# Performance work log

Hardware: AMD Instinct MI355X
Metric: run time of the kernel (lower is better)

## Reference

```python
import math
import jax, jax.numpy as jnp
import numpy as np

B, S, D, H = 2, 2048, 2048, 16
HD = D // H
INV_NORM = 1.0 / math.sqrt(HD)


def _build_alibi(batch, n_heads, seq_len):
    # Standard BLOOM ALiBi slopes (n_heads is a power of two here)
    base = 2.0 ** (-(2.0 ** -(math.log2(n_heads) - 3)))
    slopes = base ** np.arange(1, n_heads + 1, dtype=np.float32)  # [H]
    pos = np.arange(seq_len, dtype=np.float32)  # [S]
    alibi = slopes[:, None] * pos[None, :]  # [H, S]
    alibi = np.broadcast_to(alibi[None], (batch, n_heads, seq_len)).reshape(batch * n_heads, 1, seq_len)
    return jnp.asarray(alibi)


def _build_causal_mask(batch, seq_len):
    neg = jnp.float32(-1e9)
    tril = jnp.tril(jnp.ones((seq_len, seq_len), dtype=bool))
    mask = jnp.where(tril, jnp.float32(0.0), neg)  # [S, S]
    return jnp.broadcast_to(mask[None, None], (batch, 1, seq_len, seq_len))


def setup_inputs() -> dict:
    key = jax.random.key(0)
    ks = jax.random.split(key, 6)
    scale = 0.02
    return {
        "hidden_states": jax.random.normal(ks[0], (B, S, D), jnp.float32),
        "residual": jax.random.normal(ks[1], (B, S, D), jnp.float32),
        "alibi": _build_alibi(B, H, S),
        "attention_mask": _build_causal_mask(B, S),
        "W_qkv": jax.random.normal(ks[2], (3 * D, D), jnp.float32) * scale,
        "b_qkv": jax.random.normal(ks[3], (3 * D,), jnp.float32) * scale,
        "W_dense": jax.random.normal(ks[4], (D, D), jnp.float32) * scale,
        "b_dense": jax.random.normal(ks[5], (D,), jnp.float32) * scale,
    }


def reference(hidden_states, residual, alibi, attention_mask, W_qkv, b_qkv, W_dense, b_dense):
    b, s, d = hidden_states.shape
    # fused QKV projection: [B,S,3D] -> [B,S,H,3,HD]
    fused = (hidden_states @ W_qkv.T + b_qkv).reshape(b, s, H, 3, HD)
    q = fused[..., 0, :].transpose(0, 2, 1, 3)  # [B,H,S,HD]
    k = fused[..., 1, :].transpose(0, 2, 1, 3)
    v = fused[..., 2, :].transpose(0, 2, 1, 3)
    # baddbmm: alibi + inv_norm * q @ k^T ; alibi is [B*H,1,S] -> broadcast over q_len
    scores = alibi.reshape(b, H, 1, s) + INV_NORM * jnp.einsum("bhqd,bhkd->bhqk", q, k)
    scores = scores + attention_mask  # additive causal mask [B,1,S,S]
    probs = jax.nn.softmax(scores.astype(jnp.float32), axis=-1).astype(hidden_states.dtype)
    ctx = jnp.einsum("bhqk,bhkd->bhqd", probs, v)  # [B,H,S,HD]
    ctx = ctx.transpose(0, 2, 1, 3).reshape(b, s, d)  # merge heads
    out = ctx @ W_dense.T + b_dense
    return out + residual  # dropout_add with p=0 (eval)
```

## Files before the change

kernel.cpp:

```cpp
#include <hip/hip_runtime.h>
#include <hip/hip_bf16.h>

typedef __hip_bfloat16 bf16;
typedef __attribute__((ext_vector_type(8))) short s8v;
typedef __attribute__((ext_vector_type(4))) float f4v;

#define B_  2
#define S_  2048
#define D_  2048
#define H_  16
#define HD_ 128
#define INV_NORM 0.08838834764831845f

static __device__ __forceinline__ f4v mfma16(s8v a, s8v b, f4v c) {
    return __builtin_amdgcn_mfma_f32_16x16x32_bf16(a, b, c, 0, 0, 0);
}

static __device__ __forceinline__ void gload_lds(const void* gp, void* lp) {
    __builtin_amdgcn_global_load_lds(
        (const __attribute__((address_space(1))) unsigned int*)gp,
        (__attribute__((address_space(3))) unsigned int*)lp, 16, 0, 0);
}

__global__ __launch_bounds__(256)
void cvt_f32_bf16(const float* __restrict__ src, bf16* __restrict__ dst, int n4)
{
    int i = blockIdx.x * 256 + threadIdx.x;
    if (i < n4) {
        float4 f = ((const float4*)src)[i];
        union { ushort4 u4; bf16 h[4]; } p;
        p.h[0] = __float2bfloat16(f.x);
        p.h[1] = __float2bfloat16(f.y);
        p.h[2] = __float2bfloat16(f.z);
        p.h[3] = __float2bfloat16(f.w);
        ((ushort4*)dst)[i] = p.u4;
    }
}

template <int MODE>
__global__ __launch_bounds__(256)
void gemm_bt(const bf16* __restrict__ A, const bf16* __restrict__ Bw,
             const float* __restrict__ bias, const float* __restrict__ resid,
             bf16* __restrict__ o0, bf16* __restrict__ o1, bf16* __restrict__ o2,
             float* __restrict__ of, int K)
{
    __shared__ __align__(16) bf16 Al[128][32];
    __shared__ __align__(16) bf16 Bl[128][32];
    const int tid  = threadIdx.x;
    const int wave = tid >> 6, lane = tid & 63;
    const int col  = lane & 15, quad = lane >> 4;
    const int wm = (wave >> 1) << 6, wn = (wave & 1) << 6;
    const int bn = blockIdx.x, bm = blockIdx.y;
    const bf16* Ab = A  + (size_t)bm * 128 * K;
    const bf16* Bb = Bw + (size_t)bn * 128 * K;

    const f4v fzero = {0.f, 0.f, 0.f, 0.f};
    f4v acc[4][4];
#pragma unroll
    for (int i = 0; i < 4; i++)
#pragma unroll
        for (int j = 0; j < 4; j++) acc[i][j] = fzero;

    for (int k0 = 0; k0 < K; k0 += 32) {
#pragma unroll
        for (int p = 0; p < 2; p++) {
            const int g = p * 256 + tid;
            const int r = g >> 2, ko = (g & 3) << 3;
            gload_lds(Ab + (size_t)r * K + k0 + ko, (char*)&Al[0][0] + (size_t)g * 16);
            gload_lds(Bb + (size_t)r * K + k0 + ko, (char*)&Bl[0][0] + (size_t)g * 16);
        }
        __syncthreads();
        s8v af[4], bfr[4];
#pragma unroll
        for (int i = 0; i < 4; i++) af[i]  = *(const s8v*)&Al[wm + i * 16 + col][quad * 8];
#pragma unroll
        for (int j = 0; j < 4; j++) bfr[j] = *(const s8v*)&Bl[wn + j * 16 + col][quad * 8];
#pragma unroll
        for (int i = 0; i < 4; i++)
#pragma unroll
            for (int j = 0; j < 4; j++)
                acc[i][j] = mfma16(af[i], bfr[j], acc[i][j]);
        __syncthreads();
    }

    if (MODE == 0) {
        const int t = bn % 3, h = bn / 3;
#pragma unroll
        for (int j = 0; j < 4; j++) {
            const int c = wn + j * 16 + col;
            const float bv = bias[bn * 128 + c];
#pragma unroll
            for (int i = 0; i < 4; i++) {
                const int r  = (bm << 7) + wm + i * 16 + (quad << 2);
                const int bb = r >> 11, s = r & (S_ - 1);
                if (t == 2) {
                    union { ushort4 u4; bf16 hh[4]; } pk;
#pragma unroll
                    for (int rg = 0; rg < 4; rg++)
                        pk.hh[rg] = __float2bfloat16(acc[i][j][rg] + bv);
                    *(ushort4*)(o2 + ((size_t)(bb * H_ + h) * HD_ + c) * S_ + s) = pk.u4;
                } else {
                    bf16* dst = (t == 0) ? o0 : o1;
#pragma unroll
                    for (int rg = 0; rg < 4; rg++)
                        dst[((size_t)(bb * H_ + h) * S_ + (s + rg)) * HD_ + c] =
                            __float2bfloat16(acc[i][j][rg] + bv);
                }
            }
        }
    } else {
#pragma unroll
        for (int j = 0; j < 4; j++) {
            const int c = (bn << 7) + wn + j * 16 + col;
            const float bv = bias[c];
#pragma unroll
            for (int i = 0; i < 4; i++) {
                const int r = (bm << 7) + wm + i * 16 + (quad << 2);
#pragma unroll
                for (int rg = 0; rg < 4; rg++) {
                    const size_t idx = (size_t)(r + rg) * D_ + c;
                    of[idx] = acc[i][j][rg] + bv + resid[idx];
                }
            }
        }
    }
}

__global__ __launch_bounds__(256, 2)
void attn(const bf16* __restrict__ Qb, const bf16* __restrict__ Kb,
          const bf16* __restrict__ Vt, bf16* __restrict__ ctx)
{
    __shared__ __align__(16) char Ksm[2][64 * 256];
    __shared__ __align__(16) char Vsm[2][128 * 128];
    __shared__ __align__(16) char Pl[4 * 16 * 128];

    const int x = blockIdx.x;
    const int bh = blockIdx.y;
    const int u = (bh >> 3) & 1;
    const int qb = u ? x : (int)gridDim.x - 1 - x;
    const int b = bh >> 4, h = bh & 15;
    const int tid = threadIdx.x;
    const int wave = tid >> 6, lane = tid & 63;
    const int col = lane & 15, quad = lane >> 4;
    const int q0 = qb << 6;
    const int qg = q0 + wave * 16 + col;
    const float slope = exp2f(-0.5f * (float)(h + 1));
    const int sw = (col & 7) << 4;

    const bf16* Qp = Qb + ((size_t)bh * S_ + q0 + wave * 16) * HD_;
    s8v aq[4];
#pragma unroll
    for (int c = 0; c < 4; c++)
        aq[c] = *(const s8v*)(Qp + (size_t)col * HD_ + c * 32 + quad * 8);

    const f4v fzero = {0.f, 0.f, 0.f, 0.f};
    f4v o[8];
#pragma unroll
    for (int t = 0; t < 8; t++) o[t] = fzero;
    float m = -1e30f, l = 0.f;

    const bf16* Kbase = Kb + (size_t)bh * S_ * HD_;
    const bf16* Vbase = Vt + (size_t)bh * HD_ * S_;

    int ksrc[4], vsrc[4];
#pragma unroll
    for (int p = 0; p < 4; p++) {
        const int g = p * 256 + tid;
        const int kr = g >> 4, kb = g & 15;
        ksrc[p] = kr * HD_ + ((kb ^ (kr & 7)) << 3);
        const int vr = g >> 3, vb = g & 7;
        vsrc[p] = vr * S_ + ((vb ^ (vr & 7)) << 3);
    }
    const int ldst = tid << 4;

    {
        const bf16* Kp = Kbase;
        const bf16* Vp = Vbase;
#pragma unroll
        for (int p = 0; p < 4; p++) {
            gload_lds(Kp + ksrc[p], Ksm[0] + p * 4096 + ldst);
            gload_lds(Vp + vsrc[p], Vsm[0] + p * 4096 + ldst);
        }
    }
    __syncthreads();

    const int nkt = qb + 1;
    for (int kt = 0; kt < nkt; kt++) {
        const int cur = kt & 1;
        const int k0 = kt << 6;

        if (kt + 1 < nkt) {
            const bf16* Kp = Kbase + (size_t)(kt + 1) * 64 * HD_;
            const bf16* Vp = Vbase + (kt + 1) * 64;
            char* Kd = Ksm[cur ^ 1];
            char* Vd = Vsm[cur ^ 1];
#pragma unroll
            for (int p = 0; p < 4; p++) {
                gload_lds(Kp + ksrc[p], Kd + p * 4096 + ldst);
                gload_lds(Vp + vsrc[p], Vd + p * 4096 + ldst);
            }
        }
        const char* Kcur = Ksm[cur];
        const char* Vcur = Vsm[cur];

        f4v sc[4];
        __builtin_amdgcn_s_setprio(1);
#pragma unroll
        for (int st = 0; st < 4; st++) {
            sc[st] = fzero;
#pragma unroll
            for (int c = 0; c < 4; c++) {
                const s8v kf = *(const s8v*)(Kcur + (st * 16 + col) * 256 +
                                             ((c * 64 + quad * 16) ^ sw));
                sc[st] = mfma16(kf, aq[c], sc[st]);
            }
        }
        __builtin_amdgcn_s_setprio(0);

        float s[16];
        float mx = -1e30f;
#pragma unroll
        for (int st = 0; st < 4; st++)
#pragma unroll
            for (int r = 0; r < 4; r++) {
                const int key = k0 + st * 16 + (quad << 2) + r;
                float v = sc[st][r] * INV_NORM + slope * (float)key;
                v = (key > qg) ? -1e9f : v;
                s[st * 4 + r] = v;
                mx = fmaxf(mx, v);
            }
        mx = fmaxf(mx, __shfl_xor(mx, 16));
        mx = fmaxf(mx, __shfl_xor(mx, 32));
        const float nm = fmaxf(m, mx);
        float ps = 0.f;
#pragma unroll
        for (int i = 0; i < 16; i++) { s[i] = __expf(s[i] - nm); ps += s[i]; }
        ps += __shfl_xor(ps, 16);
        ps += __shfl_xor(ps, 32);
        const float alpha = __expf(m - nm);
        l = l * alpha + ps;
        m = nm;
#pragma unroll
        for (int t = 0; t < 8; t++) o[t] *= alpha;

        char* plw = Pl + wave * 2048 + col * 128;
#pragma unroll
        for (int st = 0; st < 4; st++) {
            union { ushort4 u4; bf16 hh[4]; } pk;
#pragma unroll
            for (int r = 0; r < 4; r++) pk.hh[r] = __float2bfloat16(s[st * 4 + r]);
            *(ushort4*)(plw + ((st * 32 + quad * 8) ^ sw)) = pk.u4;
        }
        const s8v pf0 = *(const s8v*)(plw + ((quad * 16) ^ sw));
        const s8v pf1 = *(const s8v*)(plw + ((64 + quad * 16) ^ sw));

        __builtin_amdgcn_s_setprio(1);
#pragma unroll
        for (int t = 0; t < 8; t++) {
            const s8v vf0 = *(const s8v*)(Vcur + (t * 16 + col) * 128 +
                                          ((quad * 16) ^ sw));
            o[t] = mfma16(vf0, pf0, o[t]);
            const s8v vf1 = *(const s8v*)(Vcur + (t * 16 + col) * 128 +
                                          ((64 + quad * 16) ^ sw));
            o[t] = mfma16(vf1, pf1, o[t]);
        }
        __builtin_amdgcn_s_setprio(0);

        __syncthreads();
    }

    const float rl = 1.0f / l;
#pragma unroll
    for (int t = 0; t < 8; t++) {
        union { ushort4 u4; bf16 hh[4]; } pk;
#pragma unroll
        for (int r = 0; r < 4; r++) pk.hh[r] = __float2bfloat16(o[t][r] * rl);
        *(ushort4*)&ctx[((size_t)(b * S_) + qg) * D_ + h * HD_ + t * 16 + (quad << 2)] =
            pk.u4;
    }
}

extern "C" void kernel_launch(void* const* d_in, const int* in_sizes, int n_in,
                              void* d_out, int out_size, void* d_ws, size_t ws_size,
                              hipStream_t stream)
{
    const float* hs    = (const float*)d_in[0];
    const float* resid = (const float*)d_in[1];
    const float* Wqkv  = (const float*)d_in[4];
    const float* bqkv  = (const float*)d_in[5];
    const float* Wd    = (const float*)d_in[6];
    const float* bd    = (const float*)d_in[7];
    float* out = (float*)d_out;

    const size_t seg  = (size_t)B_ * H_ * S_ * HD_;
    const size_t nHS  = (size_t)B_ * S_ * D_;
    const size_t nWq  = (size_t)3 * D_ * D_;
    const size_t nWd  = (size_t)D_ * D_;
    bf16* Qbuf = (bf16*)d_ws;
    bf16* Kbuf = Qbuf + seg;
    bf16* Vtb  = Kbuf + seg;
    bf16* ctx  = Vtb + seg;
    bf16* hsb  = ctx + seg;
    bf16* Wqb  = hsb + nHS;
    bf16* Wdb  = Wqb + nWq;

    cvt_f32_bf16<<<(int)(nHS / 4 + 255) / 256, 256, 0, stream>>>(hs, hsb, (int)(nHS / 4));
    cvt_f32_bf16<<<(int)(nWq / 4 + 255) / 256, 256, 0, stream>>>(Wqkv, Wqb, (int)(nWq / 4));
    cvt_f32_bf16<<<(int)(nWd / 4 + 255) / 256, 256, 0, stream>>>(Wd, Wdb, (int)(nWd / 4));

    gemm_bt<0><<<dim3(48, 32), 256, 0, stream>>>(hsb, Wqb, bqkv, nullptr,
                                                 Qbuf, Kbuf, Vtb, nullptr, 2048);
    attn<<<dim3(32, 32), 256, 0, stream>>>(Qbuf, Kbuf, Vtb, ctx);
    gemm_bt<1><<<dim3(16, 32), 256, 0, stream>>>(ctx, Wdb, bd, resid,
                                                 nullptr, nullptr, nullptr, out, 2048);
}
```

Before: 472.0 us.

## Replace QKV GEMM with 256x256-tile 8-wave kernel using pipelined LDS prefetch

Adds a dedicated QKV projection kernel that computes 256x256 output tiles per 512-thread block instead of 128x128. Global-to-LDS loads for the next K tile are interleaved with MFMA phases and paced by fine-grained vmcnt waits, and MFMA sections are wrapped with s_setprio. The block index is remapped so that consecutive blocks share rows. The goal is more operand reuse per LDS byte and better overlap of memory with compute. The cost is a 128KB LDS footprint and heavy register use, which may limit occupancy; the grid of 384 blocks also gives a coarser tail.

```diff
diff --git a/kernel.cpp b/kernel.cpp
--- a/kernel.cpp
+++ b/kernel.cpp
@@ -126,6 +126,143 @@
     }
 }
 
+#define VMW(s) asm volatile("s_waitcnt " s ::: "memory")
+#define BARR() { __builtin_amdgcn_s_barrier(); asm volatile("" ::: "memory"); }
+
+#define RD_A(dst, mibase)                                                       \
+  _Pragma("unroll") for (int mi = 0; mi < 4; ++mi) {                            \
+    dst[mi][0] = *(const s8v*)(lds + bufB + aR + (mibase + mi) * 4096 + sx0);   \
+    dst[mi][1] = *(const s8v*)(lds + bufB + aR + (mibase + mi) * 4096 + sx1);   \
+  }
+#define RD_B(njbase)                                                            \
+  _Pragma("unroll") for (int nj = 0; nj < 2; ++nj) {                            \
+    bfr[nj][0] = *(const s8v*)(lds + bufB + bRo + (njbase + nj) * 8192 + sx0);  \
+    bfr[nj][1] = *(const s8v*)(lds + bufB + bRo + (njbase + nj) * 8192 + sx1);  \
+  }
+#define MM(af, mibase, njbase)                                                  \
+  __builtin_amdgcn_s_setprio(1);                                                \
+  _Pragma("unroll") for (int mi = 0; mi < 4; ++mi)                              \
+  _Pragma("unroll") for (int nj = 0; nj < 2; ++nj) {                            \
+    acc[mibase + mi][njbase + nj] =                                             \
+        mfma16(af[mi][0], bfr[nj][0], acc[mibase + mi][njbase + nj]);           \
+    acc[mibase + mi][njbase + nj] =                                             \
+        mfma16(af[mi][1], bfr[nj][1], acc[mibase + mi][njbase + nj]);           \
+  }                                                                             \
+  __builtin_amdgcn_s_setprio(0);
+
+#define KTILE(DOPRE, VA, VB, VC)                                                \
+  {                                                                             \
+    const int bufB = cur << 16, bufN = (cur ^ 1) << 16;                         \
+    const size_t t1 = (size_t)(kt + 1) * 64;                                    \
+                          \
+    if (DOPRE) { gload_lds(gA + t1 + srcO0, lds + bufN + 0 + dst0);             \
+                 gload_lds(gA + t1 + srcO1, lds + bufN + 0 + dst1); }           \
+    VMW(VA); BARR();                                                            \
+    RD_A(a0, 0); RD_B(0);                                                       \
+    MM(a0, 0, 0);                                                               \
+                               \
+    if (DOPRE) { gload_lds(gB + t1 + srcO0, lds + bufN + 32768 + dst0);         \
+                 gload_lds(gB + t1 + srcO1, lds + bufN + 32768 + dst1); }       \
+    VMW(VB); BARR();                                                            \
+    RD_A(a1, 4);                                                                \
+    MM(a1, 4, 0);                                                               \
+                               \
+    if (DOPRE) { gload_lds(gA2 + t1 + srcO0, lds + bufN + 16384 + dst0);        \
+                 gload_lds(gA2 + t1 + srcO1, lds + bufN + 16384 + dst1); }      \
+    VMW(VC); BARR();                                                            \
+    RD_B(2);                                                                    \
+    MM(a0, 0, 2);                                                               \
+    BARR();     \
+                         \
+    if (DOPRE) { gload_lds(gB2 + t1 + srcO0, lds + bufN + 49152 + dst0);        \
+                 gload_lds(gB2 + t1 + srcO1, lds + bufN + 49152 + dst1); }      \
+    MM(a1, 4, 2);                                                               \
+  }
+
+__global__ __launch_bounds__(512, 2)
+void gemm_qkv8(const bf16* __restrict__ A, const bf16* __restrict__ Bw,
+               const float* __restrict__ bias,
+               bf16* __restrict__ o0, bf16* __restrict__ o1, bf16* __restrict__ o2)
+{
+    __shared__ __align__(16) char lds[131072];
+    const int tid  = threadIdx.x;
+    const int wave = tid >> 6, lane = tid & 63;
+    const int col  = lane & 15, quad = lane >> 4;
+    const int wr   = wave >> 2, wc = wave & 3;
+
+    int id = (int)blockIdx.y * 24 + (int)blockIdx.x;
+    id = (id & 7) * 48 + (id >> 3);
+    const int bm = id / 24, bn = id % 24;
+
+    const bf16* gA  = A  + (size_t)bm * 256 * 2048;
+    const bf16* gA2 = gA + (size_t)128 * 2048;
+    const bf16* gB  = Bw + (size_t)bn * 256 * 2048;
+    const bf16* gB2 = gB + (size_t)128 * 2048;
+
+    const int r0   = tid >> 3, bk0 = tid & 7;
+    const int srcO0 = r0 * 2048 + ((bk0 ^ (r0 & 7)) << 3);
+    const int srcO1 = srcO0 + 64 * 2048;
+    const int dst0 = tid * 16, dst1 = dst0 + 8192;
+
+    const int sx0 = ((quad ^ (col & 7)) << 4);
+    const int sx1 = (((4 + quad) ^ (col & 7)) << 4);
+    const int aR  = (wr * 16 + col) * 128;
+    const int bRo = (wc * 16 + col) * 128 + 32768;
+
+    const f4v fzero = {0.f, 0.f, 0.f, 0.f};
+    f4v acc[8][4];
+#pragma unroll
+    for (int i = 0; i < 8; i++)
+#pragma unroll
+        for (int j = 0; j < 4; j++) acc[i][j] = fzero;
+    s8v a0[4][2], a1[4][2], bfr[2][2];
+
+    gload_lds(gA  + srcO0, lds + 0     + dst0);
+    gload_lds(gA  + srcO1, lds + 0     + dst1);
+    gload_lds(gB  + srcO0, lds + 32768 + dst0);
+    gload_lds(gB  + srcO1, lds + 32768 + dst1);
+    gload_lds(gA2 + srcO0, lds + 16384 + dst0);
+    gload_lds(gA2 + srcO1, lds + 16384 + dst1);
+    gload_lds(gB2 + srcO0, lds + 49152 + dst0);
+    gload_lds(gB2 + srcO1, lds + 49152 + dst1);
+
+    int cur = 0;
+    for (int kt = 0; kt < 31; ++kt) {
+        KTILE(1, "vmcnt(6)", "vmcnt(6)", "vmcnt(6)");
+        cur ^= 1;
+    }
+    {
+        const int kt = 31;
+        KTILE(0, "vmcnt(4)", "vmcnt(2)", "vmcnt(0)");
+    }
+
+#pragma unroll
+    for (int mi = 0; mi < 8; ++mi) {
+#pragma unroll
+        for (int nj = 0; nj < 4; ++nj) {
+            const int cg = bn * 2 + (nj >> 1);
+            const int t3 = cg % 3, hh = cg / 3;
+            const int hd = (nj & 1) * 64 + wc * 16 + col;
+            const float bv = bias[cg * 128 + hd];
+            const int r = bm * 256 + mi * 32 + wr * 16 + (quad << 2);
+            const int bi = r >> 11, srow = r & (S_ - 1);
+            if (t3 == 2) {
+                union { ushort4 u4; bf16 hv[4]; } pk;
+#pragma unroll
+                for (int rg = 0; rg < 4; ++rg)
+                    pk.hv[rg] = __float2bfloat16(acc[mi][nj][rg] + bv);
+                *(ushort4*)(o2 + ((size_t)(bi * H_ + hh) * HD_ + hd) * S_ + srow) = pk.u4;
+            } else {
+                bf16* dst = (t3 == 0) ? o0 : o1;
+#pragma unroll
+                for (int rg = 0; rg < 4; ++rg)
+                    dst[((size_t)(bi * H_ + hh) * S_ + (srow + rg)) * HD_ + hd] =
+                        __float2bfloat16(acc[mi][nj][rg] + bv);
+            }
+        }
+    }
+}
+
 __global__ __launch_bounds__(256, 2)
 void attn(const bf16* __restrict__ Qb, const bf16* __restrict__ Kb,
           const bf16* __restrict__ Vt, bf16* __restrict__ ctx)
@@ -308,8 +445,7 @@
     cvt_f32_bf16<<<(int)(nWq / 4 + 255) / 256, 256, 0, stream>>>(Wqkv, Wqb, (int)(nWq / 4));
     cvt_f32_bf16<<<(int)(nWd / 4 + 255) / 256, 256, 0, stream>>>(Wd, Wdb, (int)(nWd / 4));
 
-    gemm_bt<0><<<dim3(48, 32), 256, 0, stream>>>(hsb, Wqb, bqkv, nullptr,
-                                                 Qbuf, Kbuf, Vtb, nullptr, 2048);
+    gemm_qkv8<<<dim3(24, 16), 512, 0, stream>>>(hsb, Wqb, bqkv, Qbuf, Kbuf, Vtb);
     attn<<<dim3(32, 32), 256, 0, stream>>>(Qbuf, Kbuf, Vtb, ctx);
     gemm_bt<1><<<dim3(16, 32), 256, 0, stream>>>(ctx, Wdb, bd, resid,
                                                  nullptr, nullptr, nullptr, out, 2048);
```

Result: faster. 450.7 us (-4.5%).
